# Kernel optimization log

Hardware: AMD Instinct MI355X
Metric: run time of the kernel (lower is better)

The kernel has to match this reference:

```python
import jax, jax.numpy as jnp
import numpy as np

B, T, N_EMBD = 8, 2048, 512
N_HEAD = 4
EPS = 1e-5
NEG_INF = -1e9


def setup_inputs() -> dict:
    key = jax.random.key(0)
    ks = jax.random.split(key, 10)
    x = jax.random.normal(ks[0], (B, T, N_EMBD), dtype=jnp.float32)
    # relative-position index map [t, t] into a (2t-1)-entry boolean mask table
    pos_emb = jax.random.randint(ks[1], (T, T), 0, 2 * T - 1)
    ln_w = jax.random.normal(ks[2], (N_EMBD,), dtype=jnp.float32) * 0.02 + 1.0
    ln_b = jax.random.normal(ks[3], (N_EMBD,), dtype=jnp.float32) * 0.02
    aff_w = jax.random.normal(ks[4], (N_EMBD,), dtype=jnp.float32) * 0.02 + 1.0
    aff_b = jax.random.normal(ks[5], (N_EMBD,), dtype=jnp.float32) * 0.02
    W_qkv = jax.random.normal(ks[6], (N_EMBD, 3 * N_EMBD), dtype=jnp.float32) * (N_EMBD ** -0.5)
    # boolean lookup table; True = position visible (mostly visible)
    mask_table = jax.random.uniform(ks[7], (2 * T - 1,)) > 0.2
    W_proj = jax.random.normal(ks[8], (N_EMBD, N_EMBD), dtype=jnp.float32) * (N_EMBD ** -0.5)
    return {
        "x": x, "pos_emb": pos_emb, "ln_w": ln_w, "ln_b": ln_b,
        "aff_w": aff_w, "aff_b": aff_b, "W_qkv": W_qkv,
        "mask_table": mask_table, "W_proj": W_proj,
    }


def reference(x, pos_emb, ln_w, ln_b, aff_w, aff_b, W_qkv, mask_table, W_proj):
    b, t, n = x.shape
    hd = n // N_HEAD
    # LayerNorm (mean subtract, rms normalize, affine)
    x = x - jnp.mean(x, axis=-1, keepdims=True)
    x = x * jax.lax.rsqrt(jnp.mean(x * x, axis=-1, keepdims=True) + EPS)
    x = x * ln_w + ln_b
    # extra affine (onnx initializers 7/8) then fused QKV projection
    x = x * aff_w + aff_b
    qkv = x @ W_qkv                       # [b, t, 3n]
    q, k, v = jnp.split(qkv, 3, axis=2)
    q = q.reshape(b, t, N_HEAD, hd).transpose(0, 2, 1, 3)  # [b, h, t, hd]
    k = k.reshape(b, t, N_HEAD, hd).transpose(0, 2, 1, 3)
    v = v.reshape(b, t, N_HEAD, hd).transpose(0, 2, 1, 3)
    scale = 1.0 / np.sqrt(hd).astype(np.float32)
    scores = jnp.einsum('bhqd,bhkd->bhqk', q, k) * scale   # [b, h, t, t]
    # gather-based relative-position mask: True = attend, False = mask out
    mask = mask_table[pos_emb]                             # [t, t] bool
    scores = jnp.where(mask, scores, NEG_INF)
    attn = jax.nn.softmax(scores, axis=-1)
    out = jnp.einsum('bhqk,bhkd->bhqd', attn, v)           # [b, h, t, hd]
    out = out.transpose(0, 2, 1, 3).reshape(b, t, n)
    return out @ W_proj
```

## Files before the change

### kernel.cpp

```cpp
#include <hip/hip_runtime.h>
#include <hip/hip_bf16.h>

#define T_SEQ 2048
#define NEMBD 512
#define NHEAD 4
#define HDIM  128
#define BATCH 8
#define MROWS (BATCH * T_SEQ)
#define QSCALE 0.12751744534f

typedef __attribute__((ext_vector_type(8))) short short8;
typedef __attribute__((ext_vector_type(4))) short short4v;
typedef __attribute__((ext_vector_type(4))) float f32x4;

static __device__ __forceinline__ float bf2f(unsigned short h) {
  return __uint_as_float(((unsigned int)h) << 16);
}
static __device__ __forceinline__ short f2bs(float f) {
  unsigned int u = __float_as_uint(f);
  unsigned int r = (u + 0x7FFFu + ((u >> 16) & 1u)) >> 16;
  return (short)r;
}
static __device__ __forceinline__ unsigned int pk2(float a, float b) {
  __hip_bfloat162 h = __float22bfloat162_rn(make_float2(a, b));
  return *reinterpret_cast<unsigned int*>(&h);
}
static __device__ __forceinline__ int mask_at(const void* mt, int fmt, int idx) {
  if (fmt == 0) return ((const int*)mt)[idx] != 0;
  if (fmt == 1) return ((const unsigned char*)mt)[idx] != 0;
  if (fmt == 2) return ((const float*)mt)[idx] != 0.0f;
  return ((const unsigned short*)mt)[idx] != 0;
}
static __device__ __forceinline__ int pos_at(const int* pos, int i64, size_t idx) {
  return i64 ? pos[idx * 2] : pos[idx];
}
static __device__ __forceinline__ void gload16(const void* g, void* l) {
  __builtin_amdgcn_global_load_lds((const __attribute__((address_space(1))) void*)g,
                                   (__attribute__((address_space(3))) void*)l,
                                   16, 0, 0);
}

__global__ __launch_bounds__(256) void detect_kernel(
    const unsigned int* __restrict__ mt, const unsigned int* __restrict__ posw,
    int* __restrict__ flags)
{
  __shared__ int s01, sf, sbf, szero;
  const int t = threadIdx.x;
  if (t == 0) { s01 = 1; sf = 1; sbf = 1; szero = 0; }
  __syncthreads();
  int a01 = 1, af = 1, ab = 1, zc = 0;
  for (int i = t; i < 1023; i += 256) {
    const unsigned int v = mt[i];
    if (v > 1u) a01 = 0;
    const float f = __uint_as_float(v);
    if (!(f == 0.0f || f == 1.0f)) af = 0;
    const unsigned int lo = v & 0xFFFFu, hi = v >> 16;
    if (!((lo == 0u || lo == 0x3F80u) && (hi == 0u || hi == 0x3F80u))) ab = 0;
  }
  for (int i = t; i < 512; i += 256) if (posw[2 * i + 1] == 0u) zc++;
  if (!a01) atomicAnd(&s01, 0);
  if (!af)  atomicAnd(&sf, 0);
  if (!ab)  atomicAnd(&sbf, 0);
  if (zc)   atomicAdd(&szero, zc);
  __syncthreads();
  if (t == 0) {
    flags[0] = s01 ? 0 : (sf ? 2 : (sbf ? 3 : 1));
    flags[2] = (szero > 500) ? 1 : 0;
  }
}

__global__ __launch_bounds__(256) void pack_mask_kernel(
    const int* __restrict__ pos, const void* __restrict__ mt,
    const int* __restrict__ flags, unsigned int* __restrict__ mp)
{
  const int idx = blockIdx.x * 256 + threadIdx.x;
  const int fmt = flags[0];
  const int i64 = flags[2];
  const int q = idx >> 6;
  const int wrd = idx & 63;
  const size_t base = (size_t)q * T_SEQ + wrd * 32;
  unsigned int bits = 0;
  #pragma unroll 4
  for (int j = 0; j < 32; ++j)
    bits |= (mask_at(mt, fmt, pos_at(pos, i64, base + j)) ? 1u : 0u) << j;
  mp[idx] = bits;
}

__global__ __launch_bounds__(256) void vecprep_kernel(
    const float* __restrict__ lnw, const float* __restrict__ lnb,
    const float* __restrict__ afw, const float* __restrict__ afb,
    float* __restrict__ effw, float* __restrict__ effb)
{
  const int c = blockIdx.x * 256 + threadIdx.x;
  if (c >= NEMBD) return;
  effw[c] = lnw[c] * afw[c];
  effb[c] = lnb[c] * afw[c] + afb[c];
}

__global__ __launch_bounds__(256) void wconv2_kernel(
    const float* __restrict__ Wq, const float* __restrict__ Wp,
    short* __restrict__ WqT, short* __restrict__ WpT)
{
  const int idx = blockIdx.x * 256 + threadIdx.x;
  if (idx < 1536 * 512) {
    const int n = idx >> 9, k = idx & 511;
    WqT[idx] = f2bs(Wq[(size_t)k * 1536 + n]);
  } else {
    const int j = idx - 1536 * 512;
    const int n = j >> 9, k = j & 511;
    WpT[j] = f2bs(Wp[(size_t)k * 512 + n]);
  }
}

__global__ __launch_bounds__(64) void ln_kernel(
    const float* __restrict__ x, const float* __restrict__ effw, const float* __restrict__ effb,
    short* __restrict__ xp)
{
  const int row = blockIdx.x;
  const int tid = threadIdx.x;
  const float4* p = (const float4*)(x + (size_t)row * NEMBD + tid * 8);
  const float4 a0 = p[0], a1 = p[1];
  float f[8] = {a0.x, a0.y, a0.z, a0.w, a1.x, a1.y, a1.z, a1.w};
  float s = 0.f, s2 = 0.f;
  #pragma unroll
  for (int j = 0; j < 8; ++j) { s += f[j]; s2 += f[j] * f[j]; }
  #pragma unroll
  for (int off = 1; off < 64; off <<= 1) {
    s  += __shfl_xor(s, off);
    s2 += __shfl_xor(s2, off);
  }
  const float mean = s * (1.0f / NEMBD);
  const float rstd = rsqrtf(s2 * (1.0f / NEMBD) - mean * mean + 1e-5f);
  const float4* wp = (const float4*)(effw + tid * 8);
  const float4* bp = (const float4*)(effb + tid * 8);
  const float4 w0 = wp[0], w1 = wp[1], b0 = bp[0], b1 = bp[1];
  short8 ob;
  ob[0] = f2bs((f[0] - mean) * rstd * w0.x + b0.x);
  ob[1] = f2bs((f[1] - mean) * rstd * w0.y + b0.y);
  ob[2] = f2bs((f[2] - mean) * rstd * w0.z + b0.z);
  ob[3] = f2bs((f[3] - mean) * rstd * w0.w + b0.w);
  ob[4] = f2bs((f[4] - mean) * rstd * w1.x + b1.x);
  ob[5] = f2bs((f[5] - mean) * rstd * w1.y + b1.y);
  ob[6] = f2bs((f[6] - mean) * rstd * w1.z + b1.z);
  ob[7] = f2bs((f[7] - mean) * rstd * w1.w + b1.w);
  *((short8*)(xp + (size_t)row * NEMBD + tid * 8)) = ob;
}

template<int MODE>
__global__ __launch_bounds__(256) void gemm_kernel(
    const short* __restrict__ A, const short* __restrict__ Bt,
    void* __restrict__ out0, short* __restrict__ Kp, short* __restrict__ Vt)
{
  __shared__ alignas(16) short Atile[128 * 64];
  __shared__ alignas(16) short Btile[128 * 64];
  const int tid = threadIdx.x;
  const int l = tid & 63;
  const int w = tid >> 6;
  const int m0 = blockIdx.x * 128;
  const int n0 = blockIdx.y * 128;
  const int w_r = w >> 1, w_c = w & 1;
  const int lr = l & 15, lg = l >> 4;
  f32x4 acc[4][4] = {};

  for (int kt = 0; kt < 512; kt += 64) {
    #pragma unroll
    for (int i = 0; i < 4; ++i) {
      const int c = i * 256 + tid;
      const int row = c >> 3, col8 = c & 7;
      gload16(A  + (size_t)(m0 + row) * 512 + kt + col8 * 8, Atile + (i * 256 + w * 64) * 8);
      gload16(Bt + (size_t)(n0 + row) * 512 + kt + col8 * 8, Btile + (i * 256 + w * 64) * 8);
    }
    __syncthreads();
    #pragma unroll
    for (int kk = 0; kk < 2; ++kk) {
      short8 af[4], bfm[4];
      #pragma unroll
      for (int m = 0; m < 4; ++m)
        af[m] = *(const short8*)&Atile[(w_r * 64 + m * 16 + lr) * 64 + kk * 32 + lg * 8];
      #pragma unroll
      for (int n = 0; n < 4; ++n)
        bfm[n] = *(const short8*)&Btile[(w_c * 64 + n * 16 + lr) * 64 + kk * 32 + lg * 8];
      #pragma unroll
      for (int m = 0; m < 4; ++m)
        #pragma unroll
        for (int n = 0; n < 4; ++n)
          acc[m][n] = __builtin_amdgcn_mfma_f32_16x16x32_bf16(af[m], bfm[n], acc[m][n], 0, 0, 0);
    }
    __syncthreads();
  }

  if (MODE == 1) {
    float* out = (float*)out0;
    #pragma unroll
    for (int m = 0; m < 4; ++m)
      #pragma unroll
      for (int n = 0; n < 4; ++n)
        #pragma unroll
        for (int r = 0; r < 4; ++r) {
          const int gm = m0 + w_r * 64 + m * 16 + lg * 4 + r;
          const int gn = n0 + w_c * 64 + n * 16 + lr;
          out[(size_t)gm * NEMBD + gn] = acc[m][n][r];
        }
  } else {
    const int which = n0 >> 9;
    const int h = (n0 >> 7) & 3;
    short* Qp = (short*)out0;
    #pragma unroll
    for (int m = 0; m < 4; ++m)
      #pragma unroll
      for (int n = 0; n < 4; ++n)
        #pragma unroll
        for (int r = 0; r < 4; ++r) {
          const int gm = m0 + w_r * 64 + m * 16 + lg * 4 + r;
          const int b = gm >> 11, t = gm & 2047;
          const int d = w_c * 64 + n * 16 + lr;
          const size_t bh = (size_t)((b << 2) | h);
          const float v = acc[m][n][r];
          if (which == 0)      Qp[(bh * T_SEQ + t) * HDIM + d] = f2bs(v * QSCALE);
          else if (which == 1) Kp[(bh * T_SEQ + t) * HDIM + d] = f2bs(v);
          else                 Vt[(bh * HDIM + d) * T_SEQ + t] = f2bs(v);
        }
  }
}

__global__ __launch_bounds__(512, 4) void attn_kernel(
    const short* __restrict__ Q, const short* __restrict__ Kp, const short* __restrict__ Vt,
    const unsigned int* __restrict__ maskP, short* __restrict__ O)
{
  __shared__ alignas(16) short Kt[3][32 * 128];
  __shared__ alignas(16) short Vs[3][128 * 32];
  __shared__ alignas(16) short Pw[8][16 * 40];
  const int tid = threadIdx.x;
  const int l = tid & 63;
  const int w = tid >> 6;
  const int lr = l & 15, lg = l >> 4;
  const int s7 = lr & 7;
  const int vkey = (lr >> 1) & 3;
  const int swz = ((blockIdx.x & 7) << 6) | (blockIdx.x >> 3);
  const int bh = swz >> 4;
  const int q0 = (swz & 15) * 128 + w * 16;
  const short* Qb = Q  + (size_t)bh * T_SEQ * HDIM;
  const short* Kb = Kp + (size_t)bh * T_SEQ * HDIM;
  const short* Vb = Vt + (size_t)bh * HDIM * T_SEQ;

  const int kr = tid >> 4, kc = tid & 15;
  const int vr = tid >> 2, vc = tid & 3;
  #define STAGE(b, kti) do {                                                        \
    const int kt_ = (kti) * 32;                                                     \
    gload16(Kb + (size_t)(kt_ + kr) * HDIM + (kc ^ (kr & 7)) * 8,                   \
            (char*)&Kt[b][0] + w * 1024);                                           \
    gload16(Vb + (size_t)vr * T_SEQ + kt_ + (vc ^ ((vr >> 1) & 3)) * 8,             \
            (char*)&Vs[b][0] + w * 1024);                                           \
  } while (0)

  short8 aq[4];
  #pragma unroll
  for (int kk = 0; kk < 4; ++kk)
    aq[kk] = *(const short8*)(Qb + (size_t)(q0 + lr) * HDIM + kk * 32 + lg * 8);

  float lsum = 0.f;
  f32x4 acc[8] = {};
  const size_t mrow = (size_t)(q0 + lr) * 64;

  STAGE(0, 0);
  int bc = 0, bn = 1;
  for (int kti = 0; kti < 64; ++kti) {
    if (kti + 1 < 64) {
      STAGE(bn, kti + 1);
      asm volatile("s_waitcnt vmcnt(2)" ::: "memory");
    } else {
      asm volatile("s_waitcnt vmcnt(0)" ::: "memory");
    }
    __builtin_amdgcn_sched_barrier(0);
    __builtin_amdgcn_s_barrier();
    const unsigned int mq = maskP[mrow + kti];
    f32x4 sn[2];
    __builtin_amdgcn_s_setprio(1);
    #pragma unroll
    for (int n = 0; n < 2; ++n) {
      f32x4 s = {};
      #pragma unroll
      for (int kk = 0; kk < 4; ++kk) {
        const short8 bk = *(const short8*)((char*)&Kt[bc][0]
            + (n * 16 + lr) * 256 + ((kk * 4 + lg) ^ s7) * 16);
        s = __builtin_amdgcn_mfma_f32_16x16x32_bf16(bk, aq[kk], s, 0, 0, 0);
      }
      sn[n] = s;
    }
    __builtin_amdgcn_s_setprio(0);
    #pragma unroll
    for (int n = 0; n < 2; ++n) {
      const int base = n * 16 + lg * 4;
      const float p0 = __builtin_amdgcn_exp2f(((mq >> (base + 0)) & 1) ? sn[n][0] : -1e9f);
      const float p1 = __builtin_amdgcn_exp2f(((mq >> (base + 1)) & 1) ? sn[n][1] : -1e9f);
      const float p2 = __builtin_amdgcn_exp2f(((mq >> (base + 2)) & 1) ? sn[n][2] : -1e9f);
      const float p3 = __builtin_amdgcn_exp2f(((mq >> (base + 3)) & 1) ? sn[n][3] : -1e9f);
      lsum += (p0 + p1) + (p2 + p3);
      union { short4v s4; unsigned int u[2]; } pwv;
      pwv.u[0] = pk2(p0, p1);
      pwv.u[1] = pk2(p2, p3);
      *(short4v*)&Pw[w][lr * 40 + base] = pwv.s4;
    }
    const short8 pa = *(const short8*)&Pw[w][lr * 40 + lg * 8];
    __builtin_amdgcn_s_setprio(1);
    #pragma unroll
    for (int nn = 0; nn < 8; ++nn) {
      const short8 bv = *(const short8*)((char*)&Vs[bc][0]
          + (nn * 16 + lr) * 64 + (lg ^ vkey) * 16);
      acc[nn] = __builtin_amdgcn_mfma_f32_16x16x32_bf16(pa, bv, acc[nn], 0, 0, 0);
    }
    __builtin_amdgcn_s_setprio(0);
    bc = bn;
    bn = (bn == 2) ? 0 : bn + 1;
  }
  #undef STAGE

  float s = lsum;
  s += __shfl_xor(s, 16);
  s += __shfl_xor(s, 32);
  const float rin = 1.0f / s;
  float rin4[4];
  #pragma unroll
  for (int r = 0; r < 4; ++r) rin4[r] = __shfl(rin, lg * 4 + r);
  const int b = bh >> 2, h = bh & 3;
  #pragma unroll
  for (int nn = 0; nn < 8; ++nn) {
    const int d = nn * 16 + lr;
    #pragma unroll
    for (int r = 0; r < 4; ++r) {
      const int qg = q0 + lg * 4 + r;
      O[((size_t)b * T_SEQ + qg) * NEMBD + h * HDIM + d] = f2bs(acc[nn][r] * rin4[r]);
    }
  }
}

__global__ __launch_bounds__(256) void fill_kernel(float* __restrict__ out, float v, size_t n) {
  for (size_t i = blockIdx.x * 256 + threadIdx.x; i < n; i += (size_t)gridDim.x * 256)
    out[i] = v;
}

extern "C" void kernel_launch(void* const* d_in, const int* in_sizes, int n_in,
                              void* d_out, int out_size, void* d_ws, size_t ws_size,
                              hipStream_t stream)
{
  const float* x     = (const float*)d_in[0];
  const int*   pos   = (const int*)d_in[1];
  const float* lnw   = (const float*)d_in[2];
  const float* lnb   = (const float*)d_in[3];
  const float* afw   = (const float*)d_in[4];
  const float* afb   = (const float*)d_in[5];
  const float* Wqkv  = (const float*)d_in[6];
  const void*  mtab  = d_in[7];
  const float* Wproj = (const float*)d_in[8];

  size_t off = 0;
  char* ws = (char*)d_ws;
  int* flags = (int*)(ws + off);                   off += 256;
  float* effw = (float*)(ws + off);                off += 2048;
  float* effb = (float*)(ws + off);                off += 2048;
  unsigned int* maskP = (unsigned int*)(ws + off); off += (size_t)T_SEQ * 64 * 4;
  short* Xp  = (short*)(ws + off);                 off += (size_t)MROWS * NEMBD * 2;
  short* WqT = (short*)(ws + off);                 off += (size_t)3 * NEMBD * NEMBD * 2;
  short* WpT = (short*)(ws + off);                 off += (size_t)NEMBD * NEMBD * 2;
  short* Qb  = (short*)(ws + off);                 off += (size_t)BATCH * NHEAD * T_SEQ * HDIM * 2;
  short* Kb  = (short*)(ws + off);                 off += (size_t)BATCH * NHEAD * T_SEQ * HDIM * 2;
  short* Vt  = (short*)(ws + off);                 off += (size_t)BATCH * NHEAD * T_SEQ * HDIM * 2;
  short* Ob  = Xp;

  if (ws_size < off) {
    fill_kernel<<<256, 256, 0, stream>>>((float*)d_out, (float)(ws_size >> 20), (size_t)out_size);
    return;
  }

  detect_kernel<<<1, 256, 0, stream>>>((const unsigned int*)mtab, (const unsigned int*)pos, flags);
  pack_mask_kernel<<<(T_SEQ * (T_SEQ / 32)) / 256, 256, 0, stream>>>(pos, mtab, flags, maskP);
  vecprep_kernel<<<2, 256, 0, stream>>>(lnw, lnb, afw, afb, effw, effb);
  wconv2_kernel<<<(4 * NEMBD * NEMBD) / 256, 256, 0, stream>>>(Wqkv, Wproj, WqT, WpT);
  ln_kernel<<<MROWS, 64, 0, stream>>>(x, effw, effb, Xp);
  dim3 g0(128, 12);
  gemm_kernel<0><<<g0, 256, 0, stream>>>(Xp, WqT, (void*)Qb, Kb, Vt);
  attn_kernel<<<512, 512, 0, stream>>>(Qb, Kb, Vt, maskP, Ob);
  dim3 g1(128, 4);
  gemm_kernel<1><<<g1, 256, 0, stream>>>(Ob, WpT, d_out, nullptr, nullptr);
}
```

Before: 219.8 us.

## Triple-buffer GEMM LDS tiles with XOR swizzle and block remapping

Restructures the bf16 GEMM main loop into a 3-stage LDS pipeline with BK=32. The next tile's async loads are issued before computing on the current one, and vmcnt waits replace the paired syncthreads. LDS chunks are XOR-swizzled to avoid bank conflicts, and MFMA sections run at raised wave priority. Blocks are remapped through a 1D grid swizzle that interleaves across 8 groups to change which tiles run together, at the cost of more complex indexing and a single barrier per stage, which depends on the ring depth to stay race-free.

Result: slower. 224.7 us (+2.2%).

```diff
diff --git a/kernel.cpp b/kernel.cpp
--- a/kernel.cpp
+++ b/kernel.cpp
@@ -147,47 +147,69 @@
 }
 
 template<int MODE>
-__global__ __launch_bounds__(256) void gemm_kernel(
+__global__ __launch_bounds__(256, 3) void gemm_kernel(
     const short* __restrict__ A, const short* __restrict__ Bt,
     void* __restrict__ out0, short* __restrict__ Kp, short* __restrict__ Vt)
 {
-  __shared__ alignas(16) short Atile[128 * 64];
-  __shared__ alignas(16) short Btile[128 * 64];
+  constexpr int NB = (MODE == 0) ? 12 : 4;
+  constexpr int PER = (128 * NB) / 8;
+  __shared__ alignas(16) short Atile[3][128 * 32];
+  __shared__ alignas(16) short Btile[3][128 * 32];
   const int tid = threadIdx.x;
   const int l = tid & 63;
   const int w = tid >> 6;
-  const int m0 = blockIdx.x * 128;
-  const int n0 = blockIdx.y * 128;
+  const int swz = (blockIdx.x & 7) * PER + (blockIdx.x >> 3);
+  const int m0 = (swz / NB) * 128;
+  const int n0 = (swz % NB) * 128;
   const int w_r = w >> 1, w_c = w & 1;
   const int lr = l & 15, lg = l >> 4;
+  const int key = lr & 3;
   f32x4 acc[4][4] = {};
 
-  for (int kt = 0; kt < 512; kt += 64) {
-    #pragma unroll
-    for (int i = 0; i < 4; ++i) {
-      const int c = i * 256 + tid;
-      const int row = c >> 3, col8 = c & 7;
-      gload16(A  + (size_t)(m0 + row) * 512 + kt + col8 * 8, Atile + (i * 256 + w * 64) * 8);
-      gload16(Bt + (size_t)(n0 + row) * 512 + kt + col8 * 8, Btile + (i * 256 + w * 64) * 8);
-    }
-    __syncthreads();
-    #pragma unroll
-    for (int kk = 0; kk < 2; ++kk) {
-      short8 af[4], bfm[4];
-      #pragma unroll
-      for (int m = 0; m < 4; ++m)
-        af[m] = *(const short8*)&Atile[(w_r * 64 + m * 16 + lr) * 64 + kk * 32 + lg * 8];
+  #define GSTAGE(b, kti) do {                                                   \
+    const int kt_ = (kti) * 32;                                                 \
+    _Pragma("unroll")                                                           \
+    for (int i = 0; i < 2; ++i) {                                               \
+      const int c = i * 256 + tid;                                              \
+      const int row = c >> 2, ch = c & 3;                                       \
+      gload16(A  + (size_t)(m0 + row) * 512 + kt_ + (ch ^ (row & 3)) * 8,       \
+              (char*)&Atile[b][0] + i * 4096 + w * 1024);                       \
+      gload16(Bt + (size_t)(n0 + row) * 512 + kt_ + (ch ^ (row & 3)) * 8,       \
+              (char*)&Btile[b][0] + i * 4096 + w * 1024);                       \
+    }                                                                           \
+  } while (0)
+
+  GSTAGE(0, 0);
+  int bc = 0, bn = 1;
+  for (int t = 0; t < 16; ++t) {
+    if (t + 1 < 16) {
+      GSTAGE(bn, t + 1);
+      asm volatile("s_waitcnt vmcnt(4)" ::: "memory");
+    } else {
+      asm volatile("s_waitcnt vmcnt(0)" ::: "memory");
+    }
+    __builtin_amdgcn_sched_barrier(0);
+    __builtin_amdgcn_s_barrier();
+    short8 af[4], bfm[4];
+    #pragma unroll
+    for (int m = 0; m < 4; ++m)
+      af[m] = *(const short8*)((char*)&Atile[bc][0]
+          + (w_r * 64 + m * 16 + lr) * 64 + ((lg ^ key) * 16));
+    #pragma unroll
+    for (int n = 0; n < 4; ++n)
+      bfm[n] = *(const short8*)((char*)&Btile[bc][0]
+          + (w_c * 64 + n * 16 + lr) * 64 + ((lg ^ key) * 16));
+    __builtin_amdgcn_s_setprio(1);
+    #pragma unroll
+    for (int m = 0; m < 4; ++m)
       #pragma unroll
       for (int n = 0; n < 4; ++n)
-        bfm[n] = *(const short8*)&Btile[(w_c * 64 + n * 16 + lr) * 64 + kk * 32 + lg * 8];
-      #pragma unroll
-      for (int m = 0; m < 4; ++m)
-        #pragma unroll
-        for (int n = 0; n < 4; ++n)
-          acc[m][n] = __builtin_amdgcn_mfma_f32_16x16x32_bf16(af[m], bfm[n], acc[m][n], 0, 0, 0);
-    }
-    __syncthreads();
-  }
+        acc[m][n] = __builtin_amdgcn_mfma_f32_16x16x32_bf16(af[m], bfm[n], acc[m][n], 0, 0, 0);
+    __builtin_amdgcn_s_setprio(0);
+    bc = bn;
+    bn = (bn == 2) ? 0 : bn + 1;
+  }
+  #undef GSTAGE
 
   if (MODE == 1) {
     float* out = (float*)out0;
@@ -377,9 +399,7 @@
   vecprep_kernel<<<2, 256, 0, stream>>>(lnw, lnb, afw, afb, effw, effb);
   wconv2_kernel<<<(4 * NEMBD * NEMBD) / 256, 256, 0, stream>>>(Wqkv, Wproj, WqT, WpT);
   ln_kernel<<<MROWS, 64, 0, stream>>>(x, effw, effb, Xp);
-  dim3 g0(128, 12);
-  gemm_kernel<0><<<g0, 256, 0, stream>>>(Xp, WqT, (void*)Qb, Kb, Vt);
+  gemm_kernel<0><<<1536, 256, 0, stream>>>(Xp, WqT, (void*)Qb, Kb, Vt);
   attn_kernel<<<512, 512, 0, stream>>>(Qb, Kb, Vt, maskP, Ob);
-  dim3 g1(128, 4);
-  gemm_kernel<1><<<g1, 256, 0, stream>>>(Ob, WpT, d_out, nullptr, nullptr);
-}
+  gemm_kernel<1><<<512, 256, 0, stream>>>(Ob, WpT, d_out, nullptr, nullptr);
+}
```
